# Performance work log

Hardware: AMD Instinct MI355X
Metric: run time of the kernel (lower is better)

## Reference

```python
import jax, jax.numpy as jnp
import numpy as np

B, T, I, H = 256, 2048, 2, 128


def setup_inputs() -> dict:
    key = jax.random.key(0)
    ks = jax.random.split(key, 8)
    s_ih = 1.0 / np.sqrt(H)
    x = jax.random.uniform(ks[0], (B, T, I), dtype=jnp.float32)
    lengths = jax.random.randint(ks[1], (B,), 1, T + 1, dtype=jnp.int32)
    # GRU params (PyTorch layout: gates stacked [r, z, n] -> 3H rows).
    W_ih = jax.random.uniform(ks[2], (3 * H, I), jnp.float32, -s_ih, s_ih)
    W_hh = jax.random.uniform(ks[3], (3 * H, H), jnp.float32, -s_ih, s_ih)
    # Module adds +1.0 to every GRU bias after default init.
    b_ih = jax.random.uniform(ks[4], (3 * H,), jnp.float32, -s_ih, s_ih) + 1.0
    b_hh = jax.random.uniform(ks[5], (3 * H,), jnp.float32, -s_ih, s_ih) + 1.0
    head_w = jax.random.uniform(ks[6], (1, H), jnp.float32, -s_ih, s_ih)
    head_b = jax.random.uniform(ks[7], (1,), jnp.float32, -s_ih, s_ih)
    return {"x": x, "lengths": lengths, "W_ih": W_ih, "W_hh": W_hh,
            "b_ih": b_ih, "b_hh": b_hh, "head_w": head_w, "head_b": head_b}


def _gru_forward(x, W_ih, W_hh, b_ih, b_hh):
    # Precompute input projections for all timesteps: [T, B, 3H]
    x_proj = jnp.einsum('bti,gi->tbg', x, W_ih) + b_ih

    def step(h, xp):
        gh = h @ W_hh.T + b_hh                 # [B, 3H]
        xr, xz, xn = jnp.split(xp, 3, axis=-1)
        hr, hz, hn = jnp.split(gh, 3, axis=-1)
        r = jax.nn.sigmoid(xr + hr)
        z = jax.nn.sigmoid(xz + hz)
        n = jnp.tanh(xn + r * hn)
        h_new = (1.0 - z) * n + z * h
        return h_new, h_new

    h0 = jnp.zeros((x.shape[0], W_hh.shape[1]), dtype=x.dtype)
    _, hs = jax.lax.scan(step, h0, x_proj)     # hs: [T, B, H]
    return hs


def reference(x, lengths, W_ih, W_hh, b_ih, b_hh, head_w, head_b):
    hs = _gru_forward(x, W_ih, W_hh, b_ih, b_hh)          # [T, B, H]
    # last valid hidden state per sequence (pack/pad + gather equivalent)
    last = hs[lengths - 1, jnp.arange(x.shape[0])]        # [B, H]
    return last @ head_w.T + head_b                        # [B, 1]
```

## Files before the change

### kernel.cpp

```cpp
#include <hip/hip_runtime.h>


#define BB 256
#define TT 2048
#define HH 128
#define NT 512

typedef int v4i __attribute__((ext_vector_type(4)));

__global__ __launch_bounds__(NT, 1) void gru_seq_kernel(
    const float* __restrict__ x,
    const int*   __restrict__ lengths,
    const float* __restrict__ W_ih,
    const float* __restrict__ W_hh,
    const float* __restrict__ b_ih,
    const float* __restrict__ b_hh,
    const float* __restrict__ head_w,
    const float* __restrict__ head_b,
    float* __restrict__ out)
{
    __shared__ __align__(16) float x_lds[(TT + 1) * 2];
    __shared__ __align__(16) signed char h_lds[2][HH];
    __shared__ float red[HH];

    const int tid = threadIdx.x;
    const int w    = tid >> 6;
    const int l    = tid & 63;
    const int lg   = l >> 4;
    const int m    = l & 15;
    const int rsel = m & 3;
    const int rep  = m >> 2;
    const int b  = blockIdx.x;
    const int len = lengths[b];

    const float S_RZ = -1.4426950408889634f;
    const float S_N  =  2.8853900817779268f;
    const float WMAX = 0.08838834764831845f;
    const float QW   = 127.0f / WMAX;
    const float CONV = WMAX / 16129.0f;
    const float C_RZ = S_RZ * CONV;
    const float C_N  = S_N * CONV;

    v4i afrag[3][2];
    #pragma unroll
    for (int g = 0; g < 3; ++g) {
        const float* Wr = W_hh + (size_t)(128 * g + 16 * w + m) * HH;
        #pragma unroll
        for (int c = 0; c < 2; ++c) {
            unsigned q[4];
            #pragma unroll
            for (int r = 0; r < 4; ++r) {
                q[r] = 0u;
                #pragma unroll
                for (int j = 0; j < 4; ++j) {
                    const float wv = Wr[64 * c + 16 * lg + 4 * r + j];
                    const unsigned bq = ((unsigned)fmaf(wv, QW, 256.5f)) & 0xFFu;
                    q[r] |= bq << (8 * j);
                }
            }
            afrag[g][c] = (v4i){(int)q[0], (int)q[1], (int)q[2], (int)q[3]};
        }
    }

    const int u = 16 * w + 4 * lg + rsel;
    const float cr0 = S_RZ * W_ih[u * 2];
    const float cr1 = S_RZ * W_ih[u * 2 + 1];
    const float crb = S_RZ * (b_ih[u] + b_hh[u]);
    const float cz0 = S_RZ * W_ih[(HH + u) * 2];
    const float cz1 = S_RZ * W_ih[(HH + u) * 2 + 1];
    const float czb = S_RZ * (b_ih[HH + u] + b_hh[HH + u]);
    const float cn0 = S_N * W_ih[(2 * HH + u) * 2];
    const float cn1 = S_N * W_ih[(2 * HH + u) * 2 + 1];
    const float cnbi = S_N * b_ih[2 * HH + u];
    const float cnbh = S_N * b_hh[2 * HH + u];
    const float hw   = head_w[u];

    {
        const float4* xb4 = (const float4*)(x + (size_t)b * TT * 2);
        float4* xl4 = (float4*)x_lds;
        #pragma unroll
        for (int i = tid; i < TT * 2 / 4; i += NT) xl4[i] = xb4[i];
    }
    if (tid == 0) { x_lds[TT * 2] = 0.f; x_lds[TT * 2 + 1] = 0.f; }
    for (int i = tid; i < 2 * HH; i += NT) ((signed char*)h_lds)[i] = 0;

    __syncthreads();

    float h_reg = 0.0f;
    int buf = 0;
    const float2* x2 = (const float2*)x_lds;
    float2 xt = x2[0];
    const v4i zero = {0, 0, 0, 0};

    for (int t = 0; t < len; ++t) {
        const signed char* hb = h_lds[buf];
        const v4i B0 = *(const v4i*)(hb + 16 * lg);
        const v4i B1 = *(const v4i*)(hb + 64 + 16 * lg);

        const float2 xt_next = x2[t + 1];

        const float xpr = fmaf(cr0, xt.x, fmaf(cr1, xt.y, crb));
        const float xpz = fmaf(cz0, xt.x, fmaf(cz1, xt.y, czb));
        const float xpn = fmaf(cn0, xt.x, fmaf(cn1, xt.y, cnbi));

        v4i accR, accZ, accN;
        accR = __builtin_amdgcn_mfma_i32_16x16x64_i8(afrag[0][0], B0, zero, 0, 0, 0);
        accZ = __builtin_amdgcn_mfma_i32_16x16x64_i8(afrag[1][0], B0, zero, 0, 0, 0);
        accN = __builtin_amdgcn_mfma_i32_16x16x64_i8(afrag[2][0], B0, zero, 0, 0, 0);
        accR = __builtin_amdgcn_mfma_i32_16x16x64_i8(afrag[0][1], B1, accR, 0, 0, 0);
        accZ = __builtin_amdgcn_mfma_i32_16x16x64_i8(afrag[1][1], B1, accZ, 0, 0, 0);
        accN = __builtin_amdgcn_mfma_i32_16x16x64_i8(afrag[2][1], B1, accN, 0, 0, 0);

        int sR, sZ, sN;
        #define PICK(acc, dst) do {                                      \
            const int _v01 = (rsel & 1) ? (acc)[1] : (acc)[0];           \
            const int _v23 = (rsel & 1) ? (acc)[3] : (acc)[2];           \
            (dst) = (rsel & 2) ? _v23 : _v01;                            \
        } while (0)
        PICK(accR, sR); PICK(accZ, sZ); PICK(accN, sN);
        #undef PICK

        const float ar = fmaf((float)sR, C_RZ, xpr);
        const float az = fmaf((float)sZ, C_RZ, xpz);
        const float r  = __builtin_amdgcn_rcpf(1.f + __builtin_amdgcn_exp2f(ar));
        const float z  = __builtin_amdgcn_rcpf(1.f + __builtin_amdgcn_exp2f(az));
        const float an = fmaf((float)sN, C_N, cnbh);
        const float uu = __builtin_amdgcn_exp2f(fmaf(r, an, xpn));
        const float n  = fmaf(-2.f, __builtin_amdgcn_rcpf(1.f + uu), 1.f);
        const float h_new = n + z * (h_reg - n);
        h_reg = h_new;

        if (rep == 0) {
            const unsigned hq = (unsigned)fmaf(h_new, 127.0f, 256.5f);
            h_lds[buf ^ 1][u] = (signed char)(hq & 0xFFu);
        }
        __syncthreads();
        buf ^= 1;
        xt = xt_next;
    }

    if (rep == 0) red[u] = h_reg * hw;
    __syncthreads();
    if (tid < 64) {
        float v = red[tid] + red[tid + 64];
        #pragma unroll
        for (int off = 32; off > 0; off >>= 1) v += __shfl_xor(v, off, 64);
        if (tid == 0) out[b] = v + head_b[0];
    }
}

extern "C" void kernel_launch(void* const* d_in, const int* in_sizes, int n_in,
                              void* d_out, int out_size, void* d_ws, size_t ws_size,
                              hipStream_t stream) {
    const float* x      = (const float*)d_in[0];
    const int*   len    = (const int*)  d_in[1];
    const float* W_ih   = (const float*)d_in[2];
    const float* W_hh   = (const float*)d_in[3];
    const float* b_ih   = (const float*)d_in[4];
    const float* b_hh   = (const float*)d_in[5];
    const float* head_w = (const float*)d_in[6];
    const float* head_b = (const float*)d_in[7];
    float* out = (float*)d_out;

    gru_seq_kernel<<<BB, NT, 0, stream>>>(x, len, W_ih, W_hh, b_ih, b_hh,
                                          head_w, head_b, out);
}
```

Before: 629.1 us.

## Halve block to 4 waves with each wave computing two 16-row tiles per gate

Cuts the block from 8 to 4 wavefronts. Each wave now holds six weight fragments and issues 12 int8 MFMAs per step instead of 6, covering 32 hidden units per gate. Fewer waves means a cheaper per-timestep __syncthreads barrier, at the cost of a longer per-wave MFMA chain and more register pressure. The hidden-state update is also rewritten as an fma with (1-z) and z*h, where z*h can be computed before n is ready.

```diff
diff --git a/kernel.cpp b/kernel.cpp
--- a/kernel.cpp
+++ b/kernel.cpp
@@ -4,7 +4,7 @@
 #define BB 256
 #define TT 2048
 #define HH 128
-#define NT 512
+#define NT 256
 
 typedef int v4i __attribute__((ext_vector_type(4)));
 
@@ -28,8 +28,9 @@
     const int l    = tid & 63;
     const int lg   = l >> 4;
     const int m    = l & 15;
-    const int rsel = m & 3;
-    const int rep  = m >> 2;
+    const int js   = m & 1;
+    const int rsel = (m >> 1) & 3;
+    const int rep  = m >> 3;
     const int b  = blockIdx.x;
     const int len = lengths[b];
 
@@ -41,28 +42,31 @@
     const float C_RZ = S_RZ * CONV;
     const float C_N  = S_N * CONV;
 
-    v4i afrag[3][2];
+    v4i afrag[6][2];
     #pragma unroll
     for (int g = 0; g < 3; ++g) {
-        const float* Wr = W_hh + (size_t)(128 * g + 16 * w + m) * HH;
         #pragma unroll
-        for (int c = 0; c < 2; ++c) {
-            unsigned q[4];
+        for (int jp = 0; jp < 2; ++jp) {
+            const float* Wr = W_hh + (size_t)(128 * g + 32 * w + 16 * jp + m) * HH;
             #pragma unroll
-            for (int r = 0; r < 4; ++r) {
-                q[r] = 0u;
+            for (int c = 0; c < 2; ++c) {
+                unsigned q[4];
                 #pragma unroll
-                for (int j = 0; j < 4; ++j) {
-                    const float wv = Wr[64 * c + 16 * lg + 4 * r + j];
-                    const unsigned bq = ((unsigned)fmaf(wv, QW, 256.5f)) & 0xFFu;
-                    q[r] |= bq << (8 * j);
+                for (int r = 0; r < 4; ++r) {
+                    q[r] = 0u;
+                    #pragma unroll
+                    for (int j = 0; j < 4; ++j) {
+                        const float wv = Wr[64 * c + 16 * lg + 4 * r + j];
+                        const unsigned bq = ((unsigned)fmaf(wv, QW, 256.5f)) & 0xFFu;
+                        q[r] |= bq << (8 * j);
+                    }
                 }
+                afrag[g * 2 + jp][c] = (v4i){(int)q[0], (int)q[1], (int)q[2], (int)q[3]};
             }
-            afrag[g][c] = (v4i){(int)q[0], (int)q[1], (int)q[2], (int)q[3]};
         }
     }
 
-    const int u = 16 * w + 4 * lg + rsel;
+    const int u = 32 * w + 16 * js + 4 * lg + rsel;
     const float cr0 = S_RZ * W_ih[u * 2];
     const float cr1 = S_RZ * W_ih[u * 2 + 1];
     const float crb = S_RZ * (b_ih[u] + b_hh[u]);
@@ -103,31 +107,37 @@
         const float xpz = fmaf(cz0, xt.x, fmaf(cz1, xt.y, czb));
         const float xpn = fmaf(cn0, xt.x, fmaf(cn1, xt.y, cnbi));
 
-        v4i accR, accZ, accN;
-        accR = __builtin_amdgcn_mfma_i32_16x16x64_i8(afrag[0][0], B0, zero, 0, 0, 0);
-        accZ = __builtin_amdgcn_mfma_i32_16x16x64_i8(afrag[1][0], B0, zero, 0, 0, 0);
-        accN = __builtin_amdgcn_mfma_i32_16x16x64_i8(afrag[2][0], B0, zero, 0, 0, 0);
-        accR = __builtin_amdgcn_mfma_i32_16x16x64_i8(afrag[0][1], B1, accR, 0, 0, 0);
-        accZ = __builtin_amdgcn_mfma_i32_16x16x64_i8(afrag[1][1], B1, accZ, 0, 0, 0);
-        accN = __builtin_amdgcn_mfma_i32_16x16x64_i8(afrag[2][1], B1, accN, 0, 0, 0);
+        v4i acc[6];
+        #pragma unroll
+        for (int j = 0; j < 6; ++j)
+            acc[j] = __builtin_amdgcn_mfma_i32_16x16x64_i8(afrag[j][0], B0, zero, 0, 0, 0);
+        #pragma unroll
+        for (int j = 0; j < 6; ++j)
+            acc[j] = __builtin_amdgcn_mfma_i32_16x16x64_i8(afrag[j][1], B1, acc[j], 0, 0, 0);
 
         int sR, sZ, sN;
-        #define PICK(acc, dst) do {                                      \
-            const int _v01 = (rsel & 1) ? (acc)[1] : (acc)[0];           \
-            const int _v23 = (rsel & 1) ? (acc)[3] : (acc)[2];           \
-            (dst) = (rsel & 2) ? _v23 : _v01;                            \
+        #define PICK(g, dst) do {                                            \
+            const int _a01 = (rsel & 1) ? acc[2*(g)][1]   : acc[2*(g)][0];   \
+            const int _a23 = (rsel & 1) ? acc[2*(g)][3]   : acc[2*(g)][2];   \
+            const int _va  = (rsel & 2) ? _a23 : _a01;                       \
+            const int _b01 = (rsel & 1) ? acc[2*(g)+1][1] : acc[2*(g)+1][0]; \
+            const int _b23 = (rsel & 1) ? acc[2*(g)+1][3] : acc[2*(g)+1][2]; \
+            const int _vb  = (rsel & 2) ? _b23 : _b01;                       \
+            (dst) = js ? _vb : _va;                                          \
         } while (0)
-        PICK(accR, sR); PICK(accZ, sZ); PICK(accN, sN);
+        PICK(0, sR); PICK(1, sZ); PICK(2, sN);
         #undef PICK
 
         const float ar = fmaf((float)sR, C_RZ, xpr);
         const float az = fmaf((float)sZ, C_RZ, xpz);
         const float r  = __builtin_amdgcn_rcpf(1.f + __builtin_amdgcn_exp2f(ar));
         const float z  = __builtin_amdgcn_rcpf(1.f + __builtin_amdgcn_exp2f(az));
+        const float omz = 1.f - z;
+        const float zh  = z * h_reg;
         const float an = fmaf((float)sN, C_N, cnbh);
         const float uu = __builtin_amdgcn_exp2f(fmaf(r, an, xpn));
         const float n  = fmaf(-2.f, __builtin_amdgcn_rcpf(1.f + uu), 1.f);
-        const float h_new = n + z * (h_reg - n);
+        const float h_new = fmaf(n, omz, zh);
         h_reg = h_new;
 
         if (rep == 0) {
```

Measured after the change: 680.5 us. 8.2% more time.
